# Kernel optimization log

Measured on AMD Instinct MI355X. Metric: run time of the kernel, lower is better.

## Reference

```python
import jax, jax.numpy as jnp
import numpy as np

N_NODES = 50000
N_FEAT = 128
N_EDGES = 600000
HIDDEN = 256  # hidden_dim
IN_DIM = 2 * N_FEAT
LEAKY_SLOPE = 0.01  # torch LeakyReLU default


def setup_inputs() -> dict:
    key = jax.random.key(0)
    ks = jax.random.split(key, 8)
    x = jax.random.normal(ks[0], (N_NODES, N_FEAT), dtype=jnp.float32)
    edge_index = jax.random.randint(ks[1], (2, N_EDGES), 0, N_NODES, dtype=jnp.int64 if jax.config.jax_enable_x64 else jnp.int32)
    # Linear params, torch default init scale ~ 1/sqrt(fan_in)
    def lin(k, fan_in, fan_out):
        k1, k2 = jax.random.split(k)
        bound = 1.0 / np.sqrt(fan_in)
        W = jax.random.uniform(k1, (fan_in, fan_out), minval=-bound, maxval=bound, dtype=jnp.float32)
        b = jax.random.uniform(k2, (fan_out,), minval=-bound, maxval=bound, dtype=jnp.float32)
        return W, b
    W1, b1 = lin(ks[2], IN_DIM, HIDDEN)
    W2, b2 = lin(ks[3], HIDDEN, HIDDEN // 2)
    W3, b3 = lin(ks[4], HIDDEN // 2, 1)
    return {"x": x, "edge_index": edge_index,
            "W1": W1, "b1": b1, "W2": W2, "b2": b2, "W3": W3, "b3": b3}


def reference(x, edge_index, W1, b1, W2, b2, W3, b3):
    row, col = edge_index[0], edge_index[1]
    # gather + concat: [E, 2F]
    combined = jnp.concatenate([x[row], x[col]], axis=1)
    h = jax.nn.relu(combined @ W1 + b1)               # [E, H] (dropout: eval mode, identity)
    h = jax.nn.leaky_relu(h @ W2 + b2, negative_slope=LEAKY_SLOPE)  # [E, H//2]
    out = (h @ W3 + b3).squeeze(-1)                   # [E]
    return out
```

## Files before the change

kernel.cpp:

```cpp
#include <hip/hip_runtime.h>
#include <hip/hip_bf16.h>

#define NNODES 50000
#define NFEAT  128
#define NEDGES 600000
#define HID    256
#define HID2   128
#define LEAKY  0.01f

typedef __attribute__((ext_vector_type(8))) short short8;
typedef __attribute__((ext_vector_type(4))) float floatx4;

__device__ __forceinline__ void split_bf16(float x, unsigned short& hi, unsigned short& lo) {
  union { float f; unsigned u; } a; a.f = x;
  hi = (unsigned short)(a.u >> 16);
  union { float f; unsigned u; } h; h.u = (unsigned)hi << 16;
  union { float f; unsigned u; } r; r.f = x - h.f;
  lo = (unsigned short)(r.u >> 16);
}

__device__ __forceinline__ unsigned short bf16_rne(float x) {
  union { float f; unsigned u; } a; a.f = x;
  unsigned r = a.u + 0x7FFFu + ((a.u >> 16) & 1u);
  return (unsigned short)(r >> 16);
}

__device__ __forceinline__ unsigned pack2_rne(float a, float b) {
  __hip_bfloat162 h = __float22bfloat162_rn(make_float2(a, b));
  unsigned u; __builtin_memcpy(&u, &h, 4); return u;
}

__device__ __forceinline__ float ubits2f(unsigned u) {
  union { unsigned u; float f; } c; c.u = u; return c.f;
}

__global__ __launch_bounds__(256) void pack_w(const float* __restrict__ W2,
                                              const float* __restrict__ W1,
                                              unsigned short* __restrict__ W2F,
                                              unsigned short* __restrict__ W1F) {
  const int gid = blockIdx.x * 256 + threadIdx.x;
  if (gid < 32768) {
    const int idx = gid;
    const int i  = idx & 7;
    const int l  = (idx >> 3) & 63;
    const int nf = (idx >> 9) & 7;
    const int ks = idx >> 12;
    const int k   = ks * 32 + (l >> 4) * 8 + i;
    const int col = nf * 16 + (l & 15);
    unsigned short hi, lo;
    split_bf16(W2[k * HID2 + col], hi, lo);
    W2F[idx]         = hi;
    W2F[32768 + idx] = lo;
  } else if (gid < 32768 + 65536) {
    const int idx = gid - 32768;
    const int i  = idx & 7;
    const int l  = (idx >> 3) & 63;
    const int nf = (idx >> 9) & 31;
    const int ks = idx >> 14;
    const int k = ks * 32 + (l >> 4) * 8 + i;
    const int n = nf * 16 + (l & 15);
    const float v = (n < 256) ? W1[k * HID + n] : W1[(128 + k) * HID + (n - 256)];
    unsigned short hi, lo;
    split_bf16(v, hi, lo);
    W1F[idx]         = hi;
    W1F[65536 + idx] = lo;
  }
}

__global__ __launch_bounds__(256) void pq_mfma(
    const float* __restrict__ x, const unsigned short* __restrict__ W1F,
    unsigned short* __restrict__ PQb) {
  const int bid   = blockIdx.x;
  const int nhalf = bid & 1;
  const int n0    = (bid >> 1) * 64;
  const int t     = threadIdx.x;

  __shared__ __align__(16) unsigned short xhi[64 * 128];
  __shared__ __align__(16) unsigned short xlo[64 * 128];

#pragma unroll
  for (int rep = 0; rep < 8; ++rep) {
    const int flat = rep * 1024 + t * 4;
    const int row = flat >> 7, f0 = flat & 127;
    float4 v = make_float4(0.f, 0.f, 0.f, 0.f);
    if (n0 + row < NNODES)
      v = *reinterpret_cast<const float4*>(&x[(size_t)(n0 + row) * NFEAT + f0]);
    unsigned short h[4], l[4];
    split_bf16(v.x, h[0], l[0]); split_bf16(v.y, h[1], l[1]);
    split_bf16(v.z, h[2], l[2]); split_bf16(v.w, h[3], l[3]);
    const unsigned bt = (unsigned)(row * 256) +
                        (((unsigned)(2 * f0)) ^ (((unsigned)(row & 7)) << 4));
    *reinterpret_cast<uint2*>(reinterpret_cast<char*>(xhi) + bt) =
        make_uint2((unsigned)h[0] | ((unsigned)h[1] << 16),
                   (unsigned)h[2] | ((unsigned)h[3] << 16));
    *reinterpret_cast<uint2*>(reinterpret_cast<char*>(xlo) + bt) =
        make_uint2((unsigned)l[0] | ((unsigned)l[1] << 16),
                   (unsigned)l[2] | ((unsigned)l[3] << 16));
  }
  __syncthreads();

  const int wid = t >> 6, lane = t & 63;
  const int rg = wid >> 1, cg = wid & 1;
  const int lr = lane & 15, kc = lane >> 4;

  floatx4 acc[2][8];
#pragma unroll
  for (int mf = 0; mf < 2; ++mf)
#pragma unroll
    for (int nf = 0; nf < 8; ++nf) acc[mf][nf] = (floatx4)0.f;

#pragma unroll
  for (int ks = 0; ks < 4; ++ks) {
    short8 ah[2], al[2];
#pragma unroll
    for (int mf = 0; mf < 2; ++mf) {
      const int row = rg * 32 + mf * 16 + lr;
      const unsigned bt = (unsigned)(row * 256) +
                          (((unsigned)(ks * 64 + kc * 16)) ^ (((unsigned)(row & 7)) << 4));
      ah[mf] = *reinterpret_cast<const short8*>(reinterpret_cast<const char*>(xhi) + bt);
      al[mf] = *reinterpret_cast<const short8*>(reinterpret_cast<const char*>(xlo) + bt);
    }
#pragma unroll
    for (int nf = 0; nf < 8; ++nf) {
      const int nfg = nhalf * 16 + cg * 8 + nf;
      const size_t off = ((size_t)(ks * 32 + nfg) * 64 + lane) * 8;
      const short8 bh = *reinterpret_cast<const short8*>(W1F + off);
      const short8 bl = *reinterpret_cast<const short8*>(W1F + 65536 + off);
#pragma unroll
      for (int mf = 0; mf < 2; ++mf) {
        acc[mf][nf] = __builtin_amdgcn_mfma_f32_16x16x32_bf16(ah[mf], bh, acc[mf][nf], 0, 0, 0);
        acc[mf][nf] = __builtin_amdgcn_mfma_f32_16x16x32_bf16(ah[mf], bl, acc[mf][nf], 0, 0, 0);
        acc[mf][nf] = __builtin_amdgcn_mfma_f32_16x16x32_bf16(al[mf], bh, acc[mf][nf], 0, 0, 0);
      }
    }
  }

#pragma unroll
  for (int mf = 0; mf < 2; ++mf)
#pragma unroll
    for (int nf = 0; nf < 8; ++nf)
#pragma unroll
      for (int r = 0; r < 4; ++r) {
        const int node = n0 + rg * 32 + mf * 16 + kc * 4 + r;
        const int col  = nhalf * 256 + cg * 128 + nf * 16 + lr;
        if (node < NNODES) PQb[(size_t)node * 512 + col] = bf16_rne(acc[mf][nf][r]);
      }
}

__global__ __launch_bounds__(256) void edge_mlp_mfma3(
    const int* __restrict__ ei, const float* __restrict__ b1,
    const unsigned short* __restrict__ W2F, const float* __restrict__ b2,
    const float* __restrict__ W3, const float* __restrict__ b3,
    const unsigned short* __restrict__ PQb, float* __restrict__ out) {
  const int t  = threadIdx.x;
  const int e0 = blockIdx.x * 64;
  const int wid = t >> 6, lane = t & 63;

  __shared__ __align__(16) unsigned short h1s[64 * 256];
  __shared__ float outs[4][64];

  {
    const unsigned vo = (unsigned)(lane * 8);
    const float4 b1v = *reinterpret_cast<const float4*>(&b1[4 * lane]);
    const int rv = ei[e0 + wid * 16 + (lane & 15)];
    const int cv = ei[NEDGES + e0 + wid * 16 + (lane & 15)];
    const char* PQc = reinterpret_cast<const char*>(PQb);

    uint2 P0[8], Q0[8], P1[8], Q1[8];
#pragma unroll
    for (int j = 0; j < 8; ++j) {
      const int r = __builtin_amdgcn_readlane(rv, j);
      const int c = __builtin_amdgcn_readlane(cv, j);
      P0[j] = *reinterpret_cast<const uint2*>(PQc + (size_t)r * 1024 + vo);
      Q0[j] = *reinterpret_cast<const uint2*>(PQc + (size_t)c * 1024 + 512 + vo);
    }
#pragma unroll
    for (int j = 0; j < 8; ++j) {
      const int r = __builtin_amdgcn_readlane(rv, 8 + j);
      const int c = __builtin_amdgcn_readlane(cv, 8 + j);
      P1[j] = *reinterpret_cast<const uint2*>(PQc + (size_t)r * 1024 + vo);
      Q1[j] = *reinterpret_cast<const uint2*>(PQc + (size_t)c * 1024 + 512 + vo);
    }

#pragma unroll
    for (int j = 0; j < 8; ++j) {
      const uint2 pu = P0[j], qu = Q0[j];
      const float v0 = fmaxf(ubits2f(pu.x << 16)         + ubits2f(qu.x << 16)         + b1v.x, 0.f);
      const float v1 = fmaxf(ubits2f(pu.x & 0xFFFF0000u) + ubits2f(qu.x & 0xFFFF0000u) + b1v.y, 0.f);
      const float v2 = fmaxf(ubits2f(pu.y << 16)         + ubits2f(qu.y << 16)         + b1v.z, 0.f);
      const float v3 = fmaxf(ubits2f(pu.y & 0xFFFF0000u) + ubits2f(qu.y & 0xFFFF0000u) + b1v.w, 0.f);
      const int e = wid * 16 + j;
      const unsigned bt = (unsigned)(e * 512) + (vo ^ (((unsigned)(e & 7)) << 4));
      *reinterpret_cast<uint2*>(reinterpret_cast<char*>(h1s) + bt) =
          make_uint2(pack2_rne(v0, v1), pack2_rne(v2, v3));
    }
#pragma unroll
    for (int j = 0; j < 8; ++j) {
      const uint2 pu = P1[j], qu = Q1[j];
      const float v0 = fmaxf(ubits2f(pu.x << 16)         + ubits2f(qu.x << 16)         + b1v.x, 0.f);
      const float v1 = fmaxf(ubits2f(pu.x & 0xFFFF0000u) + ubits2f(qu.x & 0xFFFF0000u) + b1v.y, 0.f);
      const float v2 = fmaxf(ubits2f(pu.y << 16)         + ubits2f(qu.y << 16)         + b1v.z, 0.f);
      const float v3 = fmaxf(ubits2f(pu.y & 0xFFFF0000u) + ubits2f(qu.y & 0xFFFF0000u) + b1v.w, 0.f);
      const int e = wid * 16 + 8 + j;
      const unsigned bt = (unsigned)(e * 512) + (vo ^ (((unsigned)(e & 7)) << 4));
      *reinterpret_cast<uint2*>(reinterpret_cast<char*>(h1s) + bt) =
          make_uint2(pack2_rne(v0, v1), pack2_rne(v2, v3));
    }
  }
  __syncthreads();

  const int lr = lane & 15, kc = lane >> 4;

  floatx4 acc[4][2];
#pragma unroll
  for (int mf = 0; mf < 4; ++mf)
#pragma unroll
    for (int nf = 0; nf < 2; ++nf) acc[mf][nf] = (floatx4)0.f;

#pragma unroll
  for (int ks = 0; ks < 8; ++ks) {
    short8 ah[4];
#pragma unroll
    for (int mf = 0; mf < 4; ++mf) {
      const int row = mf * 16 + lr;
      const unsigned bt = (unsigned)(row * 512) +
                          (((unsigned)(ks * 64 + kc * 16)) ^ (((unsigned)(row & 7)) << 4));
      ah[mf] = *reinterpret_cast<const short8*>(reinterpret_cast<const char*>(h1s) + bt);
    }
    short8 bh[2], bl[2];
#pragma unroll
    for (int nf = 0; nf < 2; ++nf) {
      const int nfg = wid * 2 + nf;
      const size_t off = ((size_t)(ks * 8 + nfg) * 64 + lane) * 8;
      bh[nf] = *reinterpret_cast<const short8*>(W2F + off);
      bl[nf] = *reinterpret_cast<const short8*>(W2F + 32768 + off);
    }
#pragma unroll
    for (int mf = 0; mf < 4; ++mf)
#pragma unroll
      for (int nf = 0; nf < 2; ++nf) {
        acc[mf][nf] = __builtin_amdgcn_mfma_f32_16x16x32_bf16(ah[mf], bh[nf], acc[mf][nf], 0, 0, 0);
        acc[mf][nf] = __builtin_amdgcn_mfma_f32_16x16x32_bf16(ah[mf], bl[nf], acc[mf][nf], 0, 0, 0);
      }
  }

  float w3v[2], b2v[2];
#pragma unroll
  for (int nf = 0; nf < 2; ++nf) {
    const int col = wid * 32 + nf * 16 + lr;
    w3v[nf] = W3[col];
    b2v[nf] = b2[col];
  }

  float part[4][4];
#pragma unroll
  for (int mf = 0; mf < 4; ++mf)
#pragma unroll
    for (int r = 0; r < 4; ++r) {
      float s = 0.f;
#pragma unroll
      for (int nf = 0; nf < 2; ++nf) {
        float h = acc[mf][nf][r] + b2v[nf];
        h = (h > 0.f) ? h : LEAKY * h;
        s = fmaf(h, w3v[nf], s);
      }
      part[mf][r] = s;
    }

#pragma unroll
  for (int m = 1; m <= 8; m <<= 1)
#pragma unroll
    for (int mf = 0; mf < 4; ++mf)
#pragma unroll
      for (int r = 0; r < 4; ++r) part[mf][r] += __shfl_xor(part[mf][r], m, 64);

  if (lr == 0) {
#pragma unroll
    for (int mf = 0; mf < 4; ++mf)
#pragma unroll
      for (int r = 0; r < 4; ++r) outs[wid][mf * 16 + kc * 4 + r] = part[mf][r];
  }
  __syncthreads();

  if (t < 64) {
    out[e0 + t] = outs[0][t] + outs[1][t] + outs[2][t] + outs[3][t] + b3[0];
  }
}

__global__ __launch_bounds__(256) void edge_mlp_direct(
    const float* __restrict__ x, const int* __restrict__ ei,
    const float* __restrict__ W1, const float* __restrict__ b1,
    const float* __restrict__ W2, const float* __restrict__ b2,
    const float* __restrict__ W3, const float* __restrict__ b3,
    float* __restrict__ out) {
  const int t  = threadIdx.x;
  const int e0 = blockIdx.x * 32;

  __shared__ __align__(16) float h1f[32 * HID];
  __shared__ int eidx[2][32];

  if (t < 32)      eidx[0][t]      = ei[e0 + t];
  else if (t < 64) eidx[1][t - 32] = ei[NEDGES + e0 + (t - 32)];
  __syncthreads();

  const float b1r = b1[t];
  __shared__ float xr[32][128];
  __shared__ float xc[32][128];
  for (int idx = t; idx < 32 * 128; idx += 256) {
    const int e = idx >> 7, f = idx & 127;
    xr[e][f] = x[(size_t)eidx[0][e] * NFEAT + f];
    xc[e][f] = x[(size_t)eidx[1][e] * NFEAT + f];
  }
  __syncthreads();
  float s[32];
#pragma unroll
  for (int e = 0; e < 32; ++e) s[e] = b1r;
  for (int f = 0; f < 128; ++f) {
    const float wr = W1[f * HID + t];
    const float wb = W1[(128 + f) * HID + t];
#pragma unroll
    for (int e = 0; e < 32; ++e)
      s[e] = fmaf(xr[e][f], wr, fmaf(xc[e][f], wb, s[e]));
  }
#pragma unroll
  for (int e = 0; e < 32; ++e) h1f[e * HID + t] = fmaxf(s[e], 0.f);
  __syncthreads();

  const int tr = t >> 5;
  const int tc = t & 31;
  float acc[4][4];
#pragma unroll
  for (int i = 0; i < 4; ++i)
#pragma unroll
    for (int j = 0; j < 4; ++j) acc[i][j] = 0.f;

  const float4* __restrict__ W2v = reinterpret_cast<const float4*>(W2);
  const float4* __restrict__ h1v = reinterpret_cast<const float4*>(h1f);
  for (int k = 0; k < HID; k += 4) {
    float4 a[4];
#pragma unroll
    for (int i = 0; i < 4; ++i) a[i] = h1v[((4 * tr + i) * HID + k) >> 2];
    float4 b[4];
#pragma unroll
    for (int kk = 0; kk < 4; ++kk) b[kk] = W2v[(k + kk) * 32 + tc];
#pragma unroll
    for (int i = 0; i < 4; ++i) {
      const float* av = reinterpret_cast<const float*>(&a[i]);
#pragma unroll
      for (int kk = 0; kk < 4; ++kk) {
        const float* bv = reinterpret_cast<const float*>(&b[kk]);
#pragma unroll
        for (int j = 0; j < 4; ++j) acc[i][j] = fmaf(av[kk], bv[j], acc[i][j]);
      }
    }
  }

  float w3r[4], b2r[4];
#pragma unroll
  for (int j = 0; j < 4; ++j) {
    w3r[j] = W3[4 * tc + j];
    b2r[j] = b2[4 * tc + j];
  }
  const float b3v = b3[0];
  float partial[4];
#pragma unroll
  for (int i = 0; i < 4; ++i) {
    float sp = 0.f;
#pragma unroll
    for (int j = 0; j < 4; ++j) {
      float h = acc[i][j] + b2r[j];
      h = (h > 0.f) ? h : LEAKY * h;
      sp = fmaf(h, w3r[j], sp);
    }
    partial[i] = sp;
  }
#pragma unroll
  for (int m = 16; m >= 1; m >>= 1)
#pragma unroll
    for (int i = 0; i < 4; ++i) partial[i] += __shfl_xor(partial[i], m, 32);
  if (tc == 0) {
#pragma unroll
    for (int i = 0; i < 4; ++i) out[e0 + 4 * tr + i] = partial[i] + b3v;
  }
}

extern "C" void kernel_launch(void* const* d_in, const int* in_sizes, int n_in,
                              void* d_out, int out_size, void* d_ws, size_t ws_size,
                              hipStream_t stream) {
  const float* x  = (const float*)d_in[0];
  const int*   ei = (const int*)d_in[1];
  const float* W1 = (const float*)d_in[2];
  const float* b1 = (const float*)d_in[3];
  const float* W2 = (const float*)d_in[4];
  const float* b2 = (const float*)d_in[5];
  const float* W3 = (const float*)d_in[6];
  const float* b3 = (const float*)d_in[7];
  float* out = (float*)d_out;

  const size_t pqb_bytes = (size_t)NNODES * 512 * 2;
  const size_t w2f_bytes = (size_t)2 * 32768 * 2;
  const size_t w1f_bytes = (size_t)2 * 65536 * 2;
  const size_t need = pqb_bytes + w2f_bytes + w1f_bytes;

  if (ws_size >= need) {
    unsigned short* PQb = (unsigned short*)d_ws;
    unsigned short* W2F = (unsigned short*)((char*)d_ws + pqb_bytes);
    unsigned short* W1F = (unsigned short*)((char*)d_ws + pqb_bytes + w2f_bytes);

    pack_w<<<(32768 + 65536 + 255) / 256, 256, 0, stream>>>(W2, W1, W2F, W1F);
    const int pq_blocks = ((NNODES + 63) / 64) * 2;
    pq_mfma<<<pq_blocks, 256, 0, stream>>>(x, W1F, PQb);
    edge_mlp_mfma3<<<NEDGES / 64, 256, 0, stream>>>(ei, b1, W2F, b2, W3, b3, PQb, out);
  } else {
    edge_mlp_direct<<<NEDGES / 32, 256, 0, stream>>>(x, ei, W1, b1, W2, b2, W3, b3, out);
  }
}
```

Before: 175.3 us.

## Fold b1 into node projections and split edge gather into two overlapped halves

```diff
diff --git a/kernel.cpp b/kernel.cpp
--- a/kernel.cpp
+++ b/kernel.cpp
@@ -32,6 +32,12 @@
 
 __device__ __forceinline__ float ubits2f(unsigned u) {
   union { unsigned u; float f; } c; c.u = u; return c.f;
+}
+
+__device__ __forceinline__ unsigned fuse2(unsigned pw, unsigned qw) {
+  const float a0 = ubits2f(pw << 16), a1 = ubits2f(pw & 0xFFFF0000u);
+  const float c0 = ubits2f(qw << 16), c1 = ubits2f(qw & 0xFFFF0000u);
+  return pack2_rne(fmaxf(a0 + c0, 0.f), fmaxf(a1 + c1, 0.f));
 }
 
 __global__ __launch_bounds__(256) void pack_w(const float* __restrict__ W2,
@@ -69,7 +75,7 @@
 
 __global__ __launch_bounds__(256) void pq_mfma(
     const float* __restrict__ x, const unsigned short* __restrict__ W1F,
-    unsigned short* __restrict__ PQb) {
+    const float* __restrict__ b1, unsigned short* __restrict__ PQb) {
   const int bid   = blockIdx.x;
   const int nhalf = bid & 1;
   const int n0    = (bid >> 1) * 64;
@@ -135,6 +141,11 @@
     }
   }
 
+  float bias[8];
+#pragma unroll
+  for (int nf = 0; nf < 8; ++nf)
+    bias[nf] = (nhalf == 0) ? b1[cg * 128 + nf * 16 + lr] : 0.f;
+
 #pragma unroll
   for (int mf = 0; mf < 2; ++mf)
 #pragma unroll
@@ -143,69 +154,50 @@
       for (int r = 0; r < 4; ++r) {
         const int node = n0 + rg * 32 + mf * 16 + kc * 4 + r;
         const int col  = nhalf * 256 + cg * 128 + nf * 16 + lr;
-        if (node < NNODES) PQb[(size_t)node * 512 + col] = bf16_rne(acc[mf][nf][r]);
-      }
-}
-
-__global__ __launch_bounds__(256) void edge_mlp_mfma3(
-    const int* __restrict__ ei, const float* __restrict__ b1,
+        if (node < NNODES)
+          PQb[(size_t)node * 512 + col] = bf16_rne(acc[mf][nf][r] + bias[nf]);
+      }
+}
+
+__global__ __launch_bounds__(256) void edge_mlp_mfma4(
+    const int* __restrict__ ei,
     const unsigned short* __restrict__ W2F, const float* __restrict__ b2,
     const float* __restrict__ W3, const float* __restrict__ b3,
     const unsigned short* __restrict__ PQb, float* __restrict__ out) {
   const int t  = threadIdx.x;
   const int e0 = blockIdx.x * 64;
   const int wid = t >> 6, lane = t & 63;
+  const int q    = lane >> 4;
+  const int vo16 = (lane & 15) * 16;
 
   __shared__ __align__(16) unsigned short h1s[64 * 256];
   __shared__ float outs[4][64];
 
-  {
-    const unsigned vo = (unsigned)(lane * 8);
-    const float4 b1v = *reinterpret_cast<const float4*>(&b1[4 * lane]);
-    const int rv = ei[e0 + wid * 16 + (lane & 15)];
-    const int cv = ei[NEDGES + e0 + wid * 16 + (lane & 15)];
-    const char* PQc = reinterpret_cast<const char*>(PQb);
-
-    uint2 P0[8], Q0[8], P1[8], Q1[8];
-#pragma unroll
-    for (int j = 0; j < 8; ++j) {
-      const int r = __builtin_amdgcn_readlane(rv, j);
-      const int c = __builtin_amdgcn_readlane(cv, j);
-      P0[j] = *reinterpret_cast<const uint2*>(PQc + (size_t)r * 1024 + vo);
-      Q0[j] = *reinterpret_cast<const uint2*>(PQc + (size_t)c * 1024 + 512 + vo);
-    }
-#pragma unroll
-    for (int j = 0; j < 8; ++j) {
-      const int r = __builtin_amdgcn_readlane(rv, 8 + j);
-      const int c = __builtin_amdgcn_readlane(cv, 8 + j);
-      P1[j] = *reinterpret_cast<const uint2*>(PQc + (size_t)r * 1024 + vo);
-      Q1[j] = *reinterpret_cast<const uint2*>(PQc + (size_t)c * 1024 + 512 + vo);
-    }
-
-#pragma unroll
-    for (int j = 0; j < 8; ++j) {
-      const uint2 pu = P0[j], qu = Q0[j];
-      const float v0 = fmaxf(ubits2f(pu.x << 16)         + ubits2f(qu.x << 16)         + b1v.x, 0.f);
-      const float v1 = fmaxf(ubits2f(pu.x & 0xFFFF0000u) + ubits2f(qu.x & 0xFFFF0000u) + b1v.y, 0.f);
-      const float v2 = fmaxf(ubits2f(pu.y << 16)         + ubits2f(qu.y << 16)         + b1v.z, 0.f);
-      const float v3 = fmaxf(ubits2f(pu.y & 0xFFFF0000u) + ubits2f(qu.y & 0xFFFF0000u) + b1v.w, 0.f);
-      const int e = wid * 16 + j;
-      const unsigned bt = (unsigned)(e * 512) + (vo ^ (((unsigned)(e & 7)) << 4));
-      *reinterpret_cast<uint2*>(reinterpret_cast<char*>(h1s) + bt) =
-          make_uint2(pack2_rne(v0, v1), pack2_rne(v2, v3));
-    }
-#pragma unroll
-    for (int j = 0; j < 8; ++j) {
-      const uint2 pu = P1[j], qu = Q1[j];
-      const float v0 = fmaxf(ubits2f(pu.x << 16)         + ubits2f(qu.x << 16)         + b1v.x, 0.f);
-      const float v1 = fmaxf(ubits2f(pu.x & 0xFFFF0000u) + ubits2f(qu.x & 0xFFFF0000u) + b1v.y, 0.f);
-      const float v2 = fmaxf(ubits2f(pu.y << 16)         + ubits2f(qu.y << 16)         + b1v.z, 0.f);
-      const float v3 = fmaxf(ubits2f(pu.y & 0xFFFF0000u) + ubits2f(qu.y & 0xFFFF0000u) + b1v.w, 0.f);
-      const int e = wid * 16 + 8 + j;
-      const unsigned bt = (unsigned)(e * 512) + (vo ^ (((unsigned)(e & 7)) << 4));
-      *reinterpret_cast<uint2*>(reinterpret_cast<char*>(h1s) + bt) =
-          make_uint2(pack2_rne(v0, v1), pack2_rne(v2, v3));
-    }
+  const int rv = ei[e0 + wid * 16 + (lane & 15)];
+  const int cv = ei[NEDGES + e0 + wid * 16 + (lane & 15)];
+  const char* PQc = reinterpret_cast<const char*>(PQb);
+
+  uint4 P0[4], P1[4], Q0[4], Q1[4];
+#pragma unroll
+  for (int it = 0; it < 4; ++it) {
+    const int r = __shfl(rv, 4 * it + q);
+    const int c = __shfl(cv, 4 * it + q);
+    const char* bp = PQc + (size_t)r * 1024 + vo16;
+    const char* bq = PQc + (size_t)c * 1024 + vo16;
+    P0[it] = *reinterpret_cast<const uint4*>(bp);
+    P1[it] = *reinterpret_cast<const uint4*>(bp + 256);
+    Q0[it] = *reinterpret_cast<const uint4*>(bq + 512);
+    Q1[it] = *reinterpret_cast<const uint4*>(bq + 768);
+  }
+
+#pragma unroll
+  for (int it = 0; it < 4; ++it) {
+    const uint4 o = make_uint4(fuse2(P0[it].x, Q0[it].x), fuse2(P0[it].y, Q0[it].y),
+                               fuse2(P0[it].z, Q0[it].z), fuse2(P0[it].w, Q0[it].w));
+    const int e = wid * 16 + 4 * it + q;
+    const unsigned bt = (unsigned)(e * 512) +
+                        (((unsigned)vo16) ^ (((unsigned)(e & 7)) << 4));
+    *reinterpret_cast<uint4*>(reinterpret_cast<char*>(h1s) + bt) = o;
   }
   __syncthreads();
 
@@ -218,7 +210,7 @@
     for (int nf = 0; nf < 2; ++nf) acc[mf][nf] = (floatx4)0.f;
 
 #pragma unroll
-  for (int ks = 0; ks < 8; ++ks) {
+  for (int ks = 0; ks < 4; ++ks) {
     short8 ah[4];
 #pragma unroll
     for (int mf = 0; mf < 4; ++mf) {
@@ -227,21 +219,53 @@
                           (((unsigned)(ks * 64 + kc * 16)) ^ (((unsigned)(row & 7)) << 4));
       ah[mf] = *reinterpret_cast<const short8*>(reinterpret_cast<const char*>(h1s) + bt);
     }
-    short8 bh[2], bl[2];
 #pragma unroll
     for (int nf = 0; nf < 2; ++nf) {
       const int nfg = wid * 2 + nf;
-      const size_t off = ((size_t)(ks * 8 + nfg) * 64 + lane) * 8;
-      bh[nf] = *reinterpret_cast<const short8*>(W2F + off);
-      bl[nf] = *reinterpret_cast<const short8*>(W2F + 32768 + off);
-    }
-#pragma unroll
-    for (int mf = 0; mf < 4; ++mf)
-#pragma unroll
-      for (int nf = 0; nf < 2; ++nf) {
-        acc[mf][nf] = __builtin_amdgcn_mfma_f32_16x16x32_bf16(ah[mf], bh[nf], acc[mf][nf], 0, 0, 0);
-        acc[mf][nf] = __builtin_amdgcn_mfma_f32_16x16x32_bf16(ah[mf], bl[nf], acc[mf][nf], 0, 0, 0);
-      }
+      const unsigned off = (unsigned)(((ks * 8 + nfg) * 64 + lane) * 8);
+      const short8 bh = *reinterpret_cast<const short8*>(W2F + off);
+      const short8 bl = *reinterpret_cast<const short8*>(W2F + 32768 + off);
+#pragma unroll
+      for (int mf = 0; mf < 4; ++mf) {
+        acc[mf][nf] = __builtin_amdgcn_mfma_f32_16x16x32_bf16(ah[mf], bh, acc[mf][nf], 0, 0, 0);
+        acc[mf][nf] = __builtin_amdgcn_mfma_f32_16x16x32_bf16(ah[mf], bl, acc[mf][nf], 0, 0, 0);
+      }
+    }
+  }
+
+#pragma unroll
+  for (int it = 0; it < 4; ++it) {
+    const uint4 o = make_uint4(fuse2(P1[it].x, Q1[it].x), fuse2(P1[it].y, Q1[it].y),
+                               fuse2(P1[it].z, Q1[it].z), fuse2(P1[it].w, Q1[it].w));
+    const int e = wid * 16 + 4 * it + q;
+    const unsigned bt = (unsigned)(e * 512) +
+                        (((unsigned)(256 + vo16)) ^ (((unsigned)(e & 7)) << 4));
+    *reinterpret_cast<uint4*>(reinterpret_cast<char*>(h1s) + bt) = o;
+  }
+  __syncthreads();
+
+#pragma unroll
+  for (int ks = 4; ks < 8; ++ks) {
+    short8 ah[4];
+#pragma unroll
+    for (int mf = 0; mf < 4; ++mf) {
+      const int row = mf * 16 + lr;
+      const unsigned bt = (unsigned)(row * 512) +
+                          (((unsigned)(ks * 64 + kc * 16)) ^ (((unsigned)(row & 7)) << 4));
+      ah[mf] = *reinterpret_cast<const short8*>(reinterpret_cast<const char*>(h1s) + bt);
+    }
+#pragma unroll
+    for (int nf = 0; nf < 2; ++nf) {
+      const int nfg = wid * 2 + nf;
+      const unsigned off = (unsigned)(((ks * 8 + nfg) * 64 + lane) * 8);
+      const short8 bh = *reinterpret_cast<const short8*>(W2F + off);
+      const short8 bl = *reinterpret_cast<const short8*>(W2F + 32768 + off);
+#pragma unroll
+      for (int mf = 0; mf < 4; ++mf) {
+        acc[mf][nf] = __builtin_amdgcn_mfma_f32_16x16x32_bf16(ah[mf], bh, acc[mf][nf], 0, 0, 0);
+        acc[mf][nf] = __builtin_amdgcn_mfma_f32_16x16x32_bf16(ah[mf], bl, acc[mf][nf], 0, 0, 0);
+      }
+    }
   }
 
   float w3v[2], b2v[2];
@@ -409,8 +433,8 @@
 
     pack_w<<<(32768 + 65536 + 255) / 256, 256, 0, stream>>>(W2, W1, W2F, W1F);
     const int pq_blocks = ((NNODES + 63) / 64) * 2;
-    pq_mfma<<<pq_blocks, 256, 0, stream>>>(x, W1F, PQb);
-    edge_mlp_mfma3<<<NEDGES / 64, 256, 0, stream>>>(ei, b1, W2F, b2, W3, b3, PQb, out);
+    pq_mfma<<<pq_blocks, 256, 0, stream>>>(x, W1F, b1, PQb);
+    edge_mlp_mfma4<<<NEDGES / 64, 256, 0, stream>>>(ei, W2F, b2, W3, b3, PQb, out);
   } else {
     edge_mlp_direct<<<NEDGES / 32, 256, 0, stream>>>(x, ei, W1, b1, W2, b2, W3, b3, out);
   }
```

New measurement: 209.0 us. +19.2%, slower.

## Make edge MLP kernel persistent over 8 tiles with register-resident W2 and prefetch

Applied to the files above, without the earlier changes.

```diff
diff --git a/kernel.cpp b/kernel.cpp
--- a/kernel.cpp
+++ b/kernel.cpp
@@ -32,6 +32,12 @@
 
 __device__ __forceinline__ float ubits2f(unsigned u) {
   union { unsigned u; float f; } c; c.u = u; return c.f;
+}
+
+__device__ __forceinline__ unsigned fuse2(unsigned pw, unsigned qw) {
+  const float a0 = ubits2f(pw << 16), a1 = ubits2f(pw & 0xFFFF0000u);
+  const float c0 = ubits2f(qw << 16), c1 = ubits2f(qw & 0xFFFF0000u);
+  return pack2_rne(fmaxf(a0 + c0, 0.f), fmaxf(a1 + c1, 0.f));
 }
 
 __global__ __launch_bounds__(256) void pack_w(const float* __restrict__ W2,
@@ -69,7 +75,7 @@
 
 __global__ __launch_bounds__(256) void pq_mfma(
     const float* __restrict__ x, const unsigned short* __restrict__ W1F,
-    unsigned short* __restrict__ PQb) {
+    const float* __restrict__ b1, unsigned short* __restrict__ PQb) {
   const int bid   = blockIdx.x;
   const int nhalf = bid & 1;
   const int n0    = (bid >> 1) * 64;
@@ -135,6 +141,11 @@
     }
   }
 
+  float bias[8];
+#pragma unroll
+  for (int nf = 0; nf < 8; ++nf)
+    bias[nf] = (nhalf == 0) ? b1[cg * 128 + nf * 16 + lr] : 0.f;
+
 #pragma unroll
   for (int mf = 0; mf < 2; ++mf)
 #pragma unroll
@@ -143,147 +154,114 @@
       for (int r = 0; r < 4; ++r) {
         const int node = n0 + rg * 32 + mf * 16 + kc * 4 + r;
         const int col  = nhalf * 256 + cg * 128 + nf * 16 + lr;
-        if (node < NNODES) PQb[(size_t)node * 512 + col] = bf16_rne(acc[mf][nf][r]);
-      }
-}
-
-__global__ __launch_bounds__(256) void edge_mlp_mfma3(
-    const int* __restrict__ ei, const float* __restrict__ b1,
+        if (node < NNODES)
+          PQb[(size_t)node * 512 + col] = bf16_rne(acc[mf][nf][r] + bias[nf]);
+      }
+}
+
+__global__ __launch_bounds__(512, 4) void edge_mlp_mfma5(
+    const int* __restrict__ ei,
     const unsigned short* __restrict__ W2F, const float* __restrict__ b2,
     const float* __restrict__ W3, const float* __restrict__ b3,
     const unsigned short* __restrict__ PQb, float* __restrict__ out) {
-  const int t  = threadIdx.x;
-  const int e0 = blockIdx.x * 64;
-  const int wid = t >> 6, lane = t & 63;
+  constexpr int T = 8;
+  constexpr int NT_TOT = NEDGES / 64;
+  const int tid  = threadIdx.x;
+  const int bid  = blockIdx.x;
+  const int wid  = tid >> 6, lane = tid & 63;
+  const int lr   = lane & 15, kc = lane >> 4;
+  const int tile0 = bid * T;
+  const int nt   = min(T, NT_TOT - tile0);
 
   __shared__ __align__(16) unsigned short h1s[64 * 256];
-  __shared__ float outs[4][64];
-
-  {
-    const unsigned vo = (unsigned)(lane * 8);
-    const float4 b1v = *reinterpret_cast<const float4*>(&b1[4 * lane]);
-    const int rv = ei[e0 + wid * 16 + (lane & 15)];
-    const int cv = ei[NEDGES + e0 + wid * 16 + (lane & 15)];
-    const char* PQc = reinterpret_cast<const char*>(PQb);
-
-    uint2 P0[8], Q0[8], P1[8], Q1[8];
+  __shared__ float outs[8][64];
+
+  const int eidx = min(tile0 * 64 + wid * 8 + (lane >> 3) * 64 + (lane & 7),
+                       NEDGES - 1);
+  const int rvAll = ei[eidx];
+  const int cvAll = ei[NEDGES + eidx];
+
+  short8 Bh[8], Bl[8];
+#pragma unroll
+  for (int ks = 0; ks < 8; ++ks) {
+    const unsigned off = (unsigned)(((ks * 8 + wid) * 64 + lane) * 8);
+    Bh[ks] = *reinterpret_cast<const short8*>(W2F + off);
+    Bl[ks] = *reinterpret_cast<const short8*>(W2F + 32768 + off);
+  }
+  const float w3v = W3[wid * 16 + lr];
+  const float b2v = b2[wid * 16 + lr];
+  const float b3v = b3[0];
+
+  const char* PQc = reinterpret_cast<const char*>(PQb);
+  const unsigned vo = (unsigned)(lane * 8);
+
+  uint2 P[8], Q[8];
+#pragma unroll
+  for (int j = 0; j < 8; ++j) {
+    const int r = __builtin_amdgcn_readlane(rvAll, j);
+    const int c = __builtin_amdgcn_readlane(cvAll, j);
+    P[j] = *reinterpret_cast<const uint2*>(PQc + (size_t)r * 1024 + vo);
+    Q[j] = *reinterpret_cast<const uint2*>(PQc + (size_t)c * 1024 + 512 + vo);
+  }
+
+  for (int t = 0; t < nt; ++t) {
 #pragma unroll
     for (int j = 0; j < 8; ++j) {
-      const int r = __builtin_amdgcn_readlane(rv, j);
-      const int c = __builtin_amdgcn_readlane(cv, j);
-      P0[j] = *reinterpret_cast<const uint2*>(PQc + (size_t)r * 1024 + vo);
-      Q0[j] = *reinterpret_cast<const uint2*>(PQc + (size_t)c * 1024 + 512 + vo);
-    }
-#pragma unroll
-    for (int j = 0; j < 8; ++j) {
-      const int r = __builtin_amdgcn_readlane(rv, 8 + j);
-      const int c = __builtin_amdgcn_readlane(cv, 8 + j);
-      P1[j] = *reinterpret_cast<const uint2*>(PQc + (size_t)r * 1024 + vo);
-      Q1[j] = *reinterpret_cast<const uint2*>(PQc + (size_t)c * 1024 + 512 + vo);
-    }
-
-#pragma unroll
-    for (int j = 0; j < 8; ++j) {
-      const uint2 pu = P0[j], qu = Q0[j];
-      const float v0 = fmaxf(ubits2f(pu.x << 16)         + ubits2f(qu.x << 16)         + b1v.x, 0.f);
-      const float v1 = fmaxf(ubits2f(pu.x & 0xFFFF0000u) + ubits2f(qu.x & 0xFFFF0000u) + b1v.y, 0.f);
-      const float v2 = fmaxf(ubits2f(pu.y << 16)         + ubits2f(qu.y << 16)         + b1v.z, 0.f);
-      const float v3 = fmaxf(ubits2f(pu.y & 0xFFFF0000u) + ubits2f(qu.y & 0xFFFF0000u) + b1v.w, 0.f);
-      const int e = wid * 16 + j;
-      const unsigned bt = (unsigned)(e * 512) + (vo ^ (((unsigned)(e & 7)) << 4));
+      const int el = wid * 8 + j;
+      const unsigned bt = (unsigned)(el * 512) + (vo ^ ((unsigned)j << 4));
       *reinterpret_cast<uint2*>(reinterpret_cast<char*>(h1s) + bt) =
-          make_uint2(pack2_rne(v0, v1), pack2_rne(v2, v3));
-    }
-#pragma unroll
-    for (int j = 0; j < 8; ++j) {
-      const uint2 pu = P1[j], qu = Q1[j];
-      const float v0 = fmaxf(ubits2f(pu.x << 16)         + ubits2f(qu.x << 16)         + b1v.x, 0.f);
-      const float v1 = fmaxf(ubits2f(pu.x & 0xFFFF0000u) + ubits2f(qu.x & 0xFFFF0000u) + b1v.y, 0.f);
-      const float v2 = fmaxf(ubits2f(pu.y << 16)         + ubits2f(qu.y << 16)         + b1v.z, 0.f);
-      const float v3 = fmaxf(ubits2f(pu.y & 0xFFFF0000u) + ubits2f(qu.y & 0xFFFF0000u) + b1v.w, 0.f);
-      const int e = wid * 16 + 8 + j;
-      const unsigned bt = (unsigned)(e * 512) + (vo ^ (((unsigned)(e & 7)) << 4));
-      *reinterpret_cast<uint2*>(reinterpret_cast<char*>(h1s) + bt) =
-          make_uint2(pack2_rne(v0, v1), pack2_rne(v2, v3));
-    }
-  }
-  __syncthreads();
-
-  const int lr = lane & 15, kc = lane >> 4;
-
-  floatx4 acc[4][2];
-#pragma unroll
-  for (int mf = 0; mf < 4; ++mf)
-#pragma unroll
-    for (int nf = 0; nf < 2; ++nf) acc[mf][nf] = (floatx4)0.f;
-
-#pragma unroll
-  for (int ks = 0; ks < 8; ++ks) {
-    short8 ah[4];
+          make_uint2(fuse2(P[j].x, Q[j].x), fuse2(P[j].y, Q[j].y));
+    }
+    __syncthreads();
+
+    if (t + 1 < nt) {
+      const int base = (t + 1) * 8;
+#pragma unroll
+      for (int j = 0; j < 8; ++j) {
+        const int r = __builtin_amdgcn_readlane(rvAll, base + j);
+        const int c = __builtin_amdgcn_readlane(cvAll, base + j);
+        P[j] = *reinterpret_cast<const uint2*>(PQc + (size_t)r * 1024 + vo);
+        Q[j] = *reinterpret_cast<const uint2*>(PQc + (size_t)c * 1024 + 512 + vo);
+      }
+    }
+
+    floatx4 acc[4];
+#pragma unroll
+    for (int mf = 0; mf < 4; ++mf) acc[mf] = (floatx4)0.f;
+#pragma unroll
+    for (int ks = 0; ks < 8; ++ks) {
+#pragma unroll
+      for (int mf = 0; mf < 4; ++mf) {
+        const int row = mf * 16 + lr;
+        const unsigned bt = (unsigned)(row * 512) +
+            (((unsigned)(ks * 64 + kc * 16)) ^ (((unsigned)(row & 7)) << 4));
+        const short8 ah = *reinterpret_cast<const short8*>(
+            reinterpret_cast<const char*>(h1s) + bt);
+        acc[mf] = __builtin_amdgcn_mfma_f32_16x16x32_bf16(ah, Bh[ks], acc[mf], 0, 0, 0);
+        acc[mf] = __builtin_amdgcn_mfma_f32_16x16x32_bf16(ah, Bl[ks], acc[mf], 0, 0, 0);
+      }
+    }
+
 #pragma unroll
     for (int mf = 0; mf < 4; ++mf) {
-      const int row = mf * 16 + lr;
-      const unsigned bt = (unsigned)(row * 512) +
-                          (((unsigned)(ks * 64 + kc * 16)) ^ (((unsigned)(row & 7)) << 4));
-      ah[mf] = *reinterpret_cast<const short8*>(reinterpret_cast<const char*>(h1s) + bt);
-    }
-    short8 bh[2], bl[2];
-#pragma unroll
-    for (int nf = 0; nf < 2; ++nf) {
-      const int nfg = wid * 2 + nf;
-      const size_t off = ((size_t)(ks * 8 + nfg) * 64 + lane) * 8;
-      bh[nf] = *reinterpret_cast<const short8*>(W2F + off);
-      bl[nf] = *reinterpret_cast<const short8*>(W2F + 32768 + off);
-    }
-#pragma unroll
-    for (int mf = 0; mf < 4; ++mf)
-#pragma unroll
-      for (int nf = 0; nf < 2; ++nf) {
-        acc[mf][nf] = __builtin_amdgcn_mfma_f32_16x16x32_bf16(ah[mf], bh[nf], acc[mf][nf], 0, 0, 0);
-        acc[mf][nf] = __builtin_amdgcn_mfma_f32_16x16x32_bf16(ah[mf], bl[nf], acc[mf][nf], 0, 0, 0);
-      }
-  }
-
-  float w3v[2], b2v[2];
-#pragma unroll
-  for (int nf = 0; nf < 2; ++nf) {
-    const int col = wid * 32 + nf * 16 + lr;
-    w3v[nf] = W3[col];
-    b2v[nf] = b2[col];
-  }
-
-  float part[4][4];
-#pragma unroll
-  for (int mf = 0; mf < 4; ++mf)
-#pragma unroll
-    for (int r = 0; r < 4; ++r) {
-      float s = 0.f;
-#pragma unroll
-      for (int nf = 0; nf < 2; ++nf) {
-        float h = acc[mf][nf][r] + b2v[nf];
+#pragma unroll
+      for (int r = 0; r < 4; ++r) {
+        float h = acc[mf][r] + b2v;
         h = (h > 0.f) ? h : LEAKY * h;
-        s = fmaf(h, w3v[nf], s);
-      }
-      part[mf][r] = s;
-    }
-
-#pragma unroll
-  for (int m = 1; m <= 8; m <<= 1)
-#pragma unroll
-    for (int mf = 0; mf < 4; ++mf)
-#pragma unroll
-      for (int r = 0; r < 4; ++r) part[mf][r] += __shfl_xor(part[mf][r], m, 64);
-
-  if (lr == 0) {
-#pragma unroll
-    for (int mf = 0; mf < 4; ++mf)
-#pragma unroll
-      for (int r = 0; r < 4; ++r) outs[wid][mf * 16 + kc * 4 + r] = part[mf][r];
-  }
-  __syncthreads();
-
-  if (t < 64) {
-    out[e0 + t] = outs[0][t] + outs[1][t] + outs[2][t] + outs[3][t] + b3[0];
+        float p = h * w3v;
+#pragma unroll
+        for (int m = 1; m <= 8; m <<= 1) p += __shfl_xor(p, m, 64);
+        if (lr == 0) outs[wid][mf * 16 + kc * 4 + r] = p;
+      }
+    }
+    __syncthreads();
+
+    if (tid < 64) {
+      float s = b3v;
+#pragma unroll
+      for (int w = 0; w < 8; ++w) s += outs[w][tid];
+      out[(tile0 + t) * 64 + tid] = s;
+    }
   }
 }
 
@@ -409,8 +387,10 @@
 
     pack_w<<<(32768 + 65536 + 255) / 256, 256, 0, stream>>>(W2, W1, W2F, W1F);
     const int pq_blocks = ((NNODES + 63) / 64) * 2;
-    pq_mfma<<<pq_blocks, 256, 0, stream>>>(x, W1F, PQb);
-    edge_mlp_mfma3<<<NEDGES / 64, 256, 0, stream>>>(ei, b1, W2F, b2, W3, b3, PQb, out);
+    pq_mfma<<<pq_blocks, 256, 0, stream>>>(x, W1F, b1, PQb);
+    const int n_tiles = NEDGES / 64;
+    const int grid = (n_tiles + 7) / 8;
+    edge_mlp_mfma5<<<grid, 512, 0, stream>>>(ei, W2F, b2, W3, b3, PQb, out);
   } else {
     edge_mlp_direct<<<NEDGES / 32, 256, 0, stream>>>(x, ei, W1, b1, W2, b2, W3, b3, out);
   }
```

Result: slower. 302.6 us (+72.6%).

## Split P/Q tables, fold bias into node GEMM, widen edge gathers to 16B

Applied to the files above, without the earlier changes.

```diff
diff --git a/kernel.cpp b/kernel.cpp
--- a/kernel.cpp
+++ b/kernel.cpp
@@ -32,6 +32,12 @@
 
 __device__ __forceinline__ float ubits2f(unsigned u) {
   union { unsigned u; float f; } c; c.u = u; return c.f;
+}
+
+__device__ __forceinline__ unsigned fuse2(unsigned pw, unsigned qw) {
+  const float a0 = ubits2f(pw << 16), a1 = ubits2f(pw & 0xFFFF0000u);
+  const float c0 = ubits2f(qw << 16), c1 = ubits2f(qw & 0xFFFF0000u);
+  return pack2_rne(fmaxf(a0 + c0, 0.f), fmaxf(a1 + c1, 0.f));
 }
 
 __global__ __launch_bounds__(256) void pack_w(const float* __restrict__ W2,
@@ -69,14 +75,16 @@
 
 __global__ __launch_bounds__(256) void pq_mfma(
     const float* __restrict__ x, const unsigned short* __restrict__ W1F,
-    unsigned short* __restrict__ PQb) {
+    const float* __restrict__ b1,
+    unsigned short* __restrict__ Pb, unsigned short* __restrict__ Qb) {
   const int bid   = blockIdx.x;
   const int nhalf = bid & 1;
   const int n0    = (bid >> 1) * 64;
   const int t     = threadIdx.x;
 
-  __shared__ __align__(16) unsigned short xhi[64 * 128];
-  __shared__ __align__(16) unsigned short xlo[64 * 128];
+  __shared__ __align__(16) unsigned short sbuf[2][64 * 128];
+  unsigned short* xhi = sbuf[0];
+  unsigned short* xlo = sbuf[1];
 
 #pragma unroll
   for (int rep = 0; rep < 8; ++rep) {
@@ -135,23 +143,44 @@
     }
   }
 
+  float bias[8];
+#pragma unroll
+  for (int nf = 0; nf < 8; ++nf)
+    bias[nf] = (nhalf == 0) ? b1[cg * 128 + nf * 16 + lr] : 0.f;
+
+  __syncthreads();
+  unsigned short* stg = &sbuf[0][0];
 #pragma unroll
   for (int mf = 0; mf < 2; ++mf)
 #pragma unroll
     for (int nf = 0; nf < 8; ++nf)
 #pragma unroll
       for (int r = 0; r < 4; ++r) {
-        const int node = n0 + rg * 32 + mf * 16 + kc * 4 + r;
-        const int col  = nhalf * 256 + cg * 128 + nf * 16 + lr;
-        if (node < NNODES) PQb[(size_t)node * 512 + col] = bf16_rne(acc[mf][nf][r]);
+        const int rl = rg * 32 + mf * 16 + kc * 4 + r;
+        const int cl = cg * 128 + nf * 16 + lr;
+        stg[rl * 256 + cl] = bf16_rne(acc[mf][nf][r] + bias[nf]);
       }
-}
-
-__global__ __launch_bounds__(256) void edge_mlp_mfma3(
-    const int* __restrict__ ei, const float* __restrict__ b1,
+  __syncthreads();
+
+  unsigned short* dst = (nhalf == 0) ? Pb : Qb;
+#pragma unroll
+  for (int rep = 0; rep < 8; ++rep) {
+    const int i = rep * 256 + t;
+    const int row = i >> 5, colu = i & 31;
+    if (n0 + row < NNODES)
+      *reinterpret_cast<uint4*>(reinterpret_cast<char*>(dst) +
+                                (size_t)(n0 + row) * 512 + colu * 16) =
+          *reinterpret_cast<const uint4*>(reinterpret_cast<const char*>(stg) +
+                                          row * 512 + colu * 16);
+  }
+}
+
+__global__ __launch_bounds__(256) void edge_mlp_mfma6(
+    const int* __restrict__ ei,
     const unsigned short* __restrict__ W2F, const float* __restrict__ b2,
     const float* __restrict__ W3, const float* __restrict__ b3,
-    const unsigned short* __restrict__ PQb, float* __restrict__ out) {
+    const unsigned short* __restrict__ Pb, const unsigned short* __restrict__ Qb,
+    float* __restrict__ out) {
   const int t  = threadIdx.x;
   const int e0 = blockIdx.x * 64;
   const int wid = t >> 6, lane = t & 63;
@@ -159,53 +188,34 @@
   __shared__ __align__(16) unsigned short h1s[64 * 256];
   __shared__ float outs[4][64];
 
-  {
-    const unsigned vo = (unsigned)(lane * 8);
-    const float4 b1v = *reinterpret_cast<const float4*>(&b1[4 * lane]);
-    const int rv = ei[e0 + wid * 16 + (lane & 15)];
-    const int cv = ei[NEDGES + e0 + wid * 16 + (lane & 15)];
-    const char* PQc = reinterpret_cast<const char*>(PQb);
-
-    uint2 P0[8], Q0[8], P1[8], Q1[8];
-#pragma unroll
-    for (int j = 0; j < 8; ++j) {
-      const int r = __builtin_amdgcn_readlane(rv, j);
-      const int c = __builtin_amdgcn_readlane(cv, j);
-      P0[j] = *reinterpret_cast<const uint2*>(PQc + (size_t)r * 1024 + vo);
-      Q0[j] = *reinterpret_cast<const uint2*>(PQc + (size_t)c * 1024 + 512 + vo);
-    }
-#pragma unroll
-    for (int j = 0; j < 8; ++j) {
-      const int r = __builtin_amdgcn_readlane(rv, 8 + j);
-      const int c = __builtin_amdgcn_readlane(cv, 8 + j);
-      P1[j] = *reinterpret_cast<const uint2*>(PQc + (size_t)r * 1024 + vo);
-      Q1[j] = *reinterpret_cast<const uint2*>(PQc + (size_t)c * 1024 + 512 + vo);
-    }
-
-#pragma unroll
-    for (int j = 0; j < 8; ++j) {
-      const uint2 pu = P0[j], qu = Q0[j];
-      const float v0 = fmaxf(ubits2f(pu.x << 16)         + ubits2f(qu.x << 16)         + b1v.x, 0.f);
-      const float v1 = fmaxf(ubits2f(pu.x & 0xFFFF0000u) + ubits2f(qu.x & 0xFFFF0000u) + b1v.y, 0.f);
-      const float v2 = fmaxf(ubits2f(pu.y << 16)         + ubits2f(qu.y << 16)         + b1v.z, 0.f);
-      const float v3 = fmaxf(ubits2f(pu.y & 0xFFFF0000u) + ubits2f(qu.y & 0xFFFF0000u) + b1v.w, 0.f);
-      const int e = wid * 16 + j;
-      const unsigned bt = (unsigned)(e * 512) + (vo ^ (((unsigned)(e & 7)) << 4));
-      *reinterpret_cast<uint2*>(reinterpret_cast<char*>(h1s) + bt) =
-          make_uint2(pack2_rne(v0, v1), pack2_rne(v2, v3));
-    }
-#pragma unroll
-    for (int j = 0; j < 8; ++j) {
-      const uint2 pu = P1[j], qu = Q1[j];
-      const float v0 = fmaxf(ubits2f(pu.x << 16)         + ubits2f(qu.x << 16)         + b1v.x, 0.f);
-      const float v1 = fmaxf(ubits2f(pu.x & 0xFFFF0000u) + ubits2f(qu.x & 0xFFFF0000u) + b1v.y, 0.f);
-      const float v2 = fmaxf(ubits2f(pu.y << 16)         + ubits2f(qu.y << 16)         + b1v.z, 0.f);
-      const float v3 = fmaxf(ubits2f(pu.y & 0xFFFF0000u) + ubits2f(qu.y & 0xFFFF0000u) + b1v.w, 0.f);
-      const int e = wid * 16 + 8 + j;
-      const unsigned bt = (unsigned)(e * 512) + (vo ^ (((unsigned)(e & 7)) << 4));
-      *reinterpret_cast<uint2*>(reinterpret_cast<char*>(h1s) + bt) =
-          make_uint2(pack2_rne(v0, v1), pack2_rne(v2, v3));
-    }
+  const int rv = ei[e0 + wid * 16 + (lane & 15)];
+  const int cv = ei[NEDGES + e0 + wid * 16 + (lane & 15)];
+  const int half = (lane >> 5) & 1;
+  const unsigned lo5 = (unsigned)(lane & 31);
+  const char* Pc = reinterpret_cast<const char*>(Pb);
+  const char* Qc = reinterpret_cast<const char*>(Qb);
+
+  uint4 Pv[8], Qv[8];
+#pragma unroll
+  for (int p = 0; p < 8; ++p) {
+    const int rlo = __builtin_amdgcn_readlane(rv, 2 * p);
+    const int rhi = __builtin_amdgcn_readlane(rv, 2 * p + 1);
+    const int clo = __builtin_amdgcn_readlane(cv, 2 * p);
+    const int chi = __builtin_amdgcn_readlane(cv, 2 * p + 1);
+    const int rr = half ? rhi : rlo;
+    const int cc = half ? chi : clo;
+    Pv[p] = *reinterpret_cast<const uint4*>(Pc + (size_t)rr * 512 + lo5 * 16);
+    Qv[p] = *reinterpret_cast<const uint4*>(Qc + (size_t)cc * 512 + lo5 * 16);
+  }
+
+#pragma unroll
+  for (int p = 0; p < 8; ++p) {
+    const uint4 o = make_uint4(fuse2(Pv[p].x, Qv[p].x), fuse2(Pv[p].y, Qv[p].y),
+                               fuse2(Pv[p].z, Qv[p].z), fuse2(Pv[p].w, Qv[p].w));
+    const int e = wid * 16 + 2 * p + half;
+    const unsigned bt = (unsigned)(e * 512) +
+                        ((lo5 * 16) ^ (((unsigned)(e & 7)) << 4));
+    *reinterpret_cast<uint4*>(reinterpret_cast<char*>(h1s) + bt) = o;
   }
   __syncthreads();
 
@@ -231,7 +241,7 @@
 #pragma unroll
     for (int nf = 0; nf < 2; ++nf) {
       const int nfg = wid * 2 + nf;
-      const size_t off = ((size_t)(ks * 8 + nfg) * 64 + lane) * 8;
+      const unsigned off = (unsigned)(((ks * 8 + nfg) * 64 + lane) * 8);
       bh[nf] = *reinterpret_cast<const short8*>(W2F + off);
       bl[nf] = *reinterpret_cast<const short8*>(W2F + 32768 + off);
     }
@@ -397,20 +407,21 @@
   const float* b3 = (const float*)d_in[7];
   float* out = (float*)d_out;
 
-  const size_t pqb_bytes = (size_t)NNODES * 512 * 2;
+  const size_t p_bytes   = (size_t)NNODES * 256 * 2;
   const size_t w2f_bytes = (size_t)2 * 32768 * 2;
   const size_t w1f_bytes = (size_t)2 * 65536 * 2;
-  const size_t need = pqb_bytes + w2f_bytes + w1f_bytes;
+  const size_t need = 2 * p_bytes + w2f_bytes + w1f_bytes;
 
   if (ws_size >= need) {
-    unsigned short* PQb = (unsigned short*)d_ws;
-    unsigned short* W2F = (unsigned short*)((char*)d_ws + pqb_bytes);
-    unsigned short* W1F = (unsigned short*)((char*)d_ws + pqb_bytes + w2f_bytes);
+    unsigned short* Pb  = (unsigned short*)d_ws;
+    unsigned short* Qb  = (unsigned short*)((char*)d_ws + p_bytes);
+    unsigned short* W2F = (unsigned short*)((char*)d_ws + 2 * p_bytes);
+    unsigned short* W1F = (unsigned short*)((char*)d_ws + 2 * p_bytes + w2f_bytes);
 
     pack_w<<<(32768 + 65536 + 255) / 256, 256, 0, stream>>>(W2, W1, W2F, W1F);
     const int pq_blocks = ((NNODES + 63) / 64) * 2;
-    pq_mfma<<<pq_blocks, 256, 0, stream>>>(x, W1F, PQb);
-    edge_mlp_mfma3<<<NEDGES / 64, 256, 0, stream>>>(ei, b1, W2F, b2, W3, b3, PQb, out);
+    pq_mfma<<<pq_blocks, 256, 0, stream>>>(x, W1F, b1, Pb, Qb);
+    edge_mlp_mfma6<<<NEDGES / 64, 256, 0, stream>>>(ei, W2F, b2, W3, b3, Pb, Qb, out);
   } else {
     edge_mlp_direct<<<NEDGES / 32, 256, 0, stream>>>(x, ei, W1, b1, W2, b2, W3, b3, out);
   }
```

Result: slower. 191.0 us (+9.0%).
